# Kernel optimization log

Measured on AMD Instinct MI355X. Metric: run time of the kernel, lower is better.

The kernel has to match this reference:

```python
import jax, jax.numpy as jnp
import numpy as np

B, S, D = 4, 2048, 768
H, E = 12, 64  # num_heads, head_size


def setup_inputs() -> dict:
    key = jax.random.key(0)
    ks = jax.random.split(key, 9)
    sd = 1.0 / np.sqrt(D)
    return {
        "x": jax.random.normal(ks[0], (B, S, D), dtype=jnp.float32),
        "Wq": jax.random.normal(ks[1], (H, D, E), dtype=jnp.float32) * sd,
        "bq": jax.random.normal(ks[2], (H, E), dtype=jnp.float32) * 0.02,
        "Wk": jax.random.normal(ks[3], (H, D, E), dtype=jnp.float32) * sd,
        "bk": jax.random.normal(ks[4], (H, E), dtype=jnp.float32) * 0.02,
        "Wv": jax.random.normal(ks[5], (H, D, E), dtype=jnp.float32) * sd,
        "bv": jax.random.normal(ks[6], (H, E), dtype=jnp.float32) * 0.02,
        "Wp": jax.random.normal(ks[7], (H * E, D), dtype=jnp.float32) * sd,
        "bp": jax.random.normal(ks[8], (D,), dtype=jnp.float32) * 0.02,
    }


def reference(x, Wq, bq, Wk, bk, Wv, bv, Wp, bp):
    # Batched multi-head QKV projections (replaces per-head Python loop)
    q = jnp.einsum("bsd,hde->bhse", x, Wq) + bq[None, :, None, :]
    k = jnp.einsum("bsd,hde->bhse", x, Wk) + bk[None, :, None, :]
    v = jnp.einsum("bsd,hde->bhse", x, Wv) + bv[None, :, None, :]
    scale = 1.0 / jnp.sqrt(jnp.asarray(E, dtype=x.dtype))
    # Full materialized attention matrix [B,H,S,S] as in the original module
    wei = jnp.einsum("bhqe,bhke->bhqk", q, k) * scale
    wei = jax.nn.softmax(wei, axis=-1)  # dropout=0 (eval) => identity
    out = jnp.einsum("bhqk,bhke->bhqe", wei, v)  # [B,H,S,E]
    # concat heads in head order then output projection
    out = out.transpose(0, 2, 1, 3).reshape(B, S, H * E)
    return out @ Wp + bp
```

## Files before the change

kernel.cpp:

```cpp
#include <hip/hip_runtime.h>
#include <cstddef>
#include <cstdint>

#define NB 4
#define NH 12
#define SQ 2048
#define DM 768
#define EH 64
#define MTOT (NB*SQ)
#define NQKV (NH*3*EH)

typedef __attribute__((ext_vector_type(8))) short short8;
typedef __attribute__((ext_vector_type(4))) float floatx4;

#define QSCALE 0.18033688011112042f

__device__ __forceinline__ unsigned short f2bf(float f) {
    unsigned int u = __float_as_uint(f);
    u += 0x7fffu + ((u >> 16) & 1u);
    return (unsigned short)(u >> 16);
}

#if __has_builtin(__builtin_amdgcn_exp2f)
__device__ __forceinline__ float fast_exp2(float x) { return __builtin_amdgcn_exp2f(x); }
#else
__device__ __forceinline__ float fast_exp2(float x) { return exp2f(x); }
#endif

#if __has_builtin(__builtin_amdgcn_cvt_pk_bf16_f32)
typedef __attribute__((ext_vector_type(2))) __bf16 bf16x2_t;
__device__ __forceinline__ unsigned int pack_bf16(float lo, float hi) {
    bf16x2_t v = __builtin_amdgcn_cvt_pk_bf16_f32(lo, hi);
    return __builtin_bit_cast(unsigned int, v);
}
#else
__device__ __forceinline__ unsigned int pack_bf16(float lo, float hi) {
    unsigned int u0 = __float_as_uint(lo) + 0x8000u;
    unsigned int u1 = __float_as_uint(hi) + 0x8000u;
    return __builtin_amdgcn_perm(u1, u0, 0x07060302u);
}
#endif
__device__ __forceinline__ short8 pack8(float a0,float a1,float a2,float a3,
                                        float b0,float b1,float b2,float b3) {
    union { unsigned int u[4]; short8 s; } cv;
    cv.u[0] = pack_bf16(a0, a1);
    cv.u[1] = pack_bf16(a2, a3);
    cv.u[2] = pack_bf16(b0, b1);
    cv.u[3] = pack_bf16(b2, b3);
    return cv.s;
}
__device__ __forceinline__ void gl_lds16(const void* g, void* l) {
    __builtin_amdgcn_global_load_lds(
        (const __attribute__((address_space(1))) unsigned int*)g,
        (__attribute__((address_space(3))) unsigned int*)l, 16, 0, 0);
}

#define CVT_A 1572864
#define CVT_BIAS (CVT_A + 576)
#define NCVT ((CVT_BIAS + 255) / 256)
__global__ __launch_bounds__(256) void convert_all(
    const float* __restrict__ x,
    const float* __restrict__ Wq, const float* __restrict__ bq,
    const float* __restrict__ Wk, const float* __restrict__ bk,
    const float* __restrict__ Wv, const float* __restrict__ bv,
    const float* __restrict__ Wp,
    unsigned short* __restrict__ Xb, unsigned short* __restrict__ Wt,
    unsigned short* __restrict__ Wpt, float* __restrict__ bias_all)
{
    __shared__ unsigned short T[64][66];
    if (blockIdx.x < NCVT) {
        int t = blockIdx.x * 256 + threadIdx.x;
        if (t < CVT_A) {
            float4 v = ((const float4*)x)[t];
            ushort4 r; r.x = f2bf(v.x); r.y = f2bf(v.y); r.z = f2bf(v.z); r.w = f2bf(v.w);
            ((ushort4*)Xb)[t] = r;
        } else if (t < CVT_BIAS) {
            int u = (t - CVT_A) * 4;
            #pragma unroll
            for (int j = 0; j < 4; j++) {
                int n = u + j;
                int h = n / 192, rr = n % 192, wsel = rr >> 6, e = rr & 63;
                const float* bs = (wsel == 0) ? bq : ((wsel == 1) ? bk : bv);
                bias_all[n] = bs[h * EH + e] * ((wsel == 0) ? QSCALE : 1.0f);
            }
        }
        return;
    }
    const int bid = blockIdx.x - NCVT;
    const int t = threadIdx.x;
    const int rr = t >> 2;
    const int c4 = (t & 3) * 16;

    const float* src; int sstride; unsigned short* dst; float sc; int kt;
    if (bid < 432) {
        int j = bid / 12; kt = bid % 12;
        int h = j / 3, wsel = j % 3;
        const float* W = (wsel == 0) ? Wq : ((wsel == 1) ? Wk : Wv);
        src = W + (size_t)h * DM * EH;
        sstride = EH;
        dst = Wt + (size_t)(h * 192 + wsel * 64) * DM;
        sc = (wsel == 0) ? QSCALE : 1.0f;
    } else {
        int u = bid - 432;
        int ni = u / 12; kt = u % 12;
        src = Wp + ni * 64;
        sstride = DM;
        dst = Wpt + (size_t)(ni * 64) * DM;
        sc = 1.0f;
    }

    const float* s = src + (size_t)(kt * 64 + rr) * sstride + c4;
    #pragma unroll
    for (int j = 0; j < 16; j++)
        T[c4 + j][rr] = f2bf(s[j] * sc);
    __syncthreads();
    uint4 d0 = *(uint4*)&T[rr][c4];
    uint4 d1 = *(uint4*)&T[rr][c4 + 8];
    *(uint4*)&dst[(size_t)rr * DM + kt * 64 + c4]     = d0;
    *(uint4*)&dst[(size_t)rr * DM + kt * 64 + c4 + 8] = d1;
}

__global__ __launch_bounds__(256, 4) void qkv_mfma(
    const unsigned short* __restrict__ Xb, const unsigned short* __restrict__ Wt,
    const float* __restrict__ bias_all,
    unsigned short* __restrict__ Qo, unsigned short* __restrict__ Kf,
    unsigned short* __restrict__ Vf)
{
    __shared__ __align__(16) unsigned short SM[16384];
    unsigned short* const As0 = SM;
    unsigned short* const Bs0 = SM + 8192;
    const int tid = threadIdx.x;
    const int w = tid >> 6, lane = tid & 63;
    const int l15 = lane & 15, quad = lane >> 4;
    const int wm = w & 1, wn = w >> 1;
    const int m0 = blockIdx.x * 128, n0 = blockIdx.y * 128;
    const int srow = w * 32 + (lane >> 2);
    const int pchunk = lane & 3;

    floatx4 acc[4][4];
    #pragma unroll
    for (int i = 0; i < 4; i++)
        #pragma unroll
        for (int j = 0; j < 4; j++) acc[i][j] = 0;

    #pragma unroll
    for (int c = 0; c < 2; c++) {
        int mr = srow + c * 16;
        int j = (pchunk - (mr >> 1)) & 3;
        gl_lds16(&Xb[(size_t)(m0 + mr) * DM + j * 8],
                 &As0[w * 1024 + c * 512 + lane * 8]);
        gl_lds16(&Wt[(size_t)(n0 + mr) * DM + j * 8],
                 &Bs0[w * 1024 + c * 512 + lane * 8]);
    }

    for (int kt = 0; kt < DM / 32; kt++) {
        const int cur = kt & 1;
        __syncthreads();
        if (kt + 1 < DM / 32) {
            int k0n = (kt + 1) * 32;
            #pragma unroll
            for (int c = 0; c < 2; c++) {
                int mr = srow + c * 16;
                int j = (pchunk - (mr >> 1)) & 3;
                gl_lds16(&Xb[(size_t)(m0 + mr) * DM + k0n + j * 8],
                         &As0[(cur ^ 1) * 4096 + w * 1024 + c * 512 + lane * 8]);
                gl_lds16(&Wt[(size_t)(n0 + mr) * DM + k0n + j * 8],
                         &Bs0[(cur ^ 1) * 4096 + w * 1024 + c * 512 + lane * 8]);
            }
        }
        short8 af[4], bf[4];
        #pragma unroll
        for (int mi = 0; mi < 4; mi++) {
            int row = wm * 64 + mi * 16 + l15;
            int pp = (quad + (row >> 1)) & 3;
            af[mi] = *(const short8*)&As0[cur * 4096 + row * 32 + pp * 8];
        }
        #pragma unroll
        for (int ni = 0; ni < 4; ni++) {
            int row = wn * 64 + ni * 16 + l15;
            int pp = (quad + (row >> 1)) & 3;
            bf[ni] = *(const short8*)&Bs0[cur * 4096 + row * 32 + pp * 8];
        }
        #pragma unroll
        for (int mi = 0; mi < 4; mi++)
            #pragma unroll
            for (int ni = 0; ni < 4; ni++)
                acc[mi][ni] = __builtin_amdgcn_mfma_f32_16x16x32_bf16(
                    af[mi], bf[ni], acc[mi][ni], 0, 0, 0);
    }
    __syncthreads();

    const int bB = m0 >> 11;
    const int ntb0 = n0 + wn * 64;
    const int h = ntb0 / 192, rr = ntb0 % 192;
    const int wsel = rr >> 6;
    const size_t bhbase = ((size_t)bB * NH + h) * (SQ * EH);
    const int sb_base = (m0 & 2047) + wm * 64;
    unsigned short* Ew = SM + w * 1152;
    float bvv[4];
    #pragma unroll
    for (int ni = 0; ni < 4; ni++) bvv[ni] = bias_all[ntb0 + ni * 16 + l15];

    if (wsel == 0) {
        #pragma unroll
        for (int mi = 0; mi < 4; mi++) {
            #pragma unroll
            for (int ni = 0; ni < 4; ni++)
                #pragma unroll
                for (int r = 0; r < 4; r++)
                    Ew[(quad * 4 + r) * 72 + ni * 16 + l15] =
                        f2bf(acc[mi][ni][r] + bvv[ni]);
            #pragma unroll
            for (int t = 0; t < 2; t++) {
                uint4 d = *(uint4*)&Ew[(t * 8 + (lane >> 3)) * 72 + (lane & 7) * 8];
                *(uint4*)&Qo[bhbase +
                    (size_t)(sb_base + mi * 16 + t * 8 + (lane >> 3)) * EH +
                    (lane & 7) * 8] = d;
            }
        }
    } else if (wsel == 1) {
        size_t tbase = bhbase + (size_t)(sb_base >> 6) * 4096;
        #pragma unroll
        for (int mi = 0; mi < 4; mi++) {
            #pragma unroll
            for (int ni = 0; ni < 4; ni++)
                #pragma unroll
                for (int r = 0; r < 4; r++)
                    Ew[(quad * 4 + r) * 72 + ni * 16 + l15] =
                        f2bf(acc[mi][ni][r] + bvv[ni]);
            #pragma unroll
            for (int t = 0; t < 2; t++) {
                uint4 d = *(uint4*)&Ew[l15 * 72 + t * 32 + quad * 8];
                *(uint4*)&Kf[tbase +
                    (size_t)((mi * 2 + t) * 64 + quad * 16 + l15) * 8] = d;
            }
        }
    } else {
        size_t tbase = bhbase + (size_t)(sb_base >> 6) * 4096;
        #pragma unroll
        for (int ni = 0; ni < 4; ni++) {
            #pragma unroll
            for (int mi = 0; mi < 4; mi++)
                #pragma unroll
                for (int r = 0; r < 4; r += 2) {
                    unsigned int pr = pack_bf16(acc[mi][ni][r]     + bvv[ni],
                                                acc[mi][ni][r + 1] + bvv[ni]);
                    *(unsigned int*)&Ew[l15 * 72 + quad * 16 + mi * 4 + r] = pr;
                }
            #pragma unroll
            for (int t = 0; t < 2; t++) {
                uint4 d = *(uint4*)&Ew[l15 * 72 + t * 32 + quad * 8];
                int unit = (ni * 2 + (quad & 1)) * 64 + ((quad >> 1) + 2 * t) * 16 + l15;
                *(uint4*)&Vf[tbase + (size_t)unit * 8] = d;
            }
        }
    }
}

__global__ __launch_bounds__(256, 3) void attn_mfma(
    const unsigned short* __restrict__ Q, const unsigned short* __restrict__ Kf,
    const unsigned short* __restrict__ Vf, unsigned short* __restrict__ O)
{
    __shared__ unsigned short Ks[3 * 4096];
    __shared__ unsigned short Vs[3 * 4096];
    const int tid = threadIdx.x;
    const int w = tid >> 6, lane = tid & 63;
    const int l15 = lane & 15, quad = lane >> 4;
    const int bh = blockIdx.x;
    const int b = bh / NH, h = bh % NH;
    const int q0 = blockIdx.y * 128;
    const int lin = blockIdx.x + gridDim.x * blockIdx.y;
    const int t0 = (lin >> 8) * 11;

    const unsigned short* Qb = Q + (size_t)bh * SQ * EH;
    const unsigned short* Kb = Kf + (size_t)bh * SQ * EH;
    const unsigned short* Vb = Vf + (size_t)bh * SQ * EH;

    short8 qf[2][2];
    #pragma unroll
    for (int qh = 0; qh < 2; qh++)
        #pragma unroll
        for (int kh = 0; kh < 2; kh++)
            qf[qh][kh] = *(const short8*)
                &Qb[(size_t)(q0 + w * 32 + qh * 16 + l15) * EH + kh * 32 + quad * 8];

    short8 ones;
    #pragma unroll
    for (int j = 0; j < 8; j++) ones[j] = (short)0x3F80;
    const floatx4 fzero = 0;

    floatx4 o[2][4], l_acc[2];
    #pragma unroll
    for (int qh = 0; qh < 2; qh++) {
        l_acc[qh] = 0;
        #pragma unroll
        for (int nb = 0; nb < 4; nb++) o[qh][nb] = 0;
    }

    const int seg = w * 2;
    {
        const unsigned short* K0 = Kb + (size_t)t0 * 4096;
        const unsigned short* V0 = Vb + (size_t)t0 * 4096;
        #pragma unroll
        for (int c = 0; c < 2; c++) {
            gl_lds16(&K0[(seg + c) * 512 + lane * 8], &Ks[(seg + c) * 512 + lane * 8]);
            gl_lds16(&V0[(seg + c) * 512 + lane * 8], &Vs[(seg + c) * 512 + lane * 8]);
        }
    }
    asm volatile("" ::: "memory");
    {
        const int t1 = (t0 + 1) & 31;
        const unsigned short* K1 = Kb + (size_t)t1 * 4096;
        const unsigned short* V1 = Vb + (size_t)t1 * 4096;
        #pragma unroll
        for (int c = 0; c < 2; c++) {
            gl_lds16(&K1[(seg + c) * 512 + lane * 8],
                     &Ks[4096 + (seg + c) * 512 + lane * 8]);
            gl_lds16(&V1[(seg + c) * 512 + lane * 8],
                     &Vs[4096 + (seg + c) * 512 + lane * 8]);
        }
    }
    asm volatile("s_waitcnt vmcnt(4)\n\ts_barrier" ::: "memory");

    int cur_off = 0;
    for (int kb = 0; kb < SQ / 64; kb++) {
        if (kb + 2 < SQ / 64) {
            int nxt_off = cur_off + 8192;
            if (nxt_off >= 12288) nxt_off -= 12288;
            const int tt2 = (t0 + kb + 2) & 31;
            const unsigned short* Kn = Kb + (size_t)tt2 * 4096;
            const unsigned short* Vn = Vb + (size_t)tt2 * 4096;
            #pragma unroll
            for (int c = 0; c < 2; c++) {
                gl_lds16(&Kn[(seg + c) * 512 + lane * 8],
                         &Ks[nxt_off + (seg + c) * 512 + lane * 8]);
                gl_lds16(&Vn[(seg + c) * 512 + lane * 8],
                         &Vs[nxt_off + (seg + c) * 512 + lane * 8]);
            }
        }

        short8 kf[4][2], vf[4][2];
        #pragma unroll
        for (int nb = 0; nb < 4; nb++)
            #pragma unroll
            for (int kh = 0; kh < 2; kh++)
                kf[nb][kh] = *(const short8*)&Ks[cur_off + ((nb * 2 + kh) * 64 + lane) * 8];
        #pragma unroll
        for (int eb = 0; eb < 4; eb++)
            #pragma unroll
            for (int kh = 0; kh < 2; kh++)
                vf[eb][kh] = *(const short8*)&Vs[cur_off + ((eb * 2 + kh) * 64 + lane) * 8];

        floatx4 s[2][4];
        __builtin_amdgcn_s_setprio(1);
        #pragma unroll
        for (int qh = 0; qh < 2; qh++)
            #pragma unroll
            for (int nb = 0; nb < 4; nb++) {
                floatx4 z = __builtin_amdgcn_mfma_f32_16x16x32_bf16(
                    kf[nb][0], qf[qh][0], fzero, 0, 0, 0);
                s[qh][nb] = __builtin_amdgcn_mfma_f32_16x16x32_bf16(
                    kf[nb][1], qf[qh][1], z, 0, 0, 0);
            }
        __builtin_amdgcn_s_setprio(0);

        short8 pa[2][2];
        #pragma unroll
        for (int qh = 0; qh < 2; qh++) {
            float p[4][4];
            #pragma unroll
            for (int nb = 0; nb < 4; nb++)
                #pragma unroll
                for (int r = 0; r < 4; r++)
                    p[nb][r] = fast_exp2(s[qh][nb][r]);
            pa[qh][0] = pack8(p[0][0], p[0][1], p[0][2], p[0][3],
                              p[1][0], p[1][1], p[1][2], p[1][3]);
            pa[qh][1] = pack8(p[2][0], p[2][1], p[2][2], p[2][3],
                              p[3][0], p[3][1], p[3][2], p[3][3]);
        }

        __builtin_amdgcn_s_setprio(1);
        #pragma unroll
        for (int qh = 0; qh < 2; qh++) {
            l_acc[qh] = __builtin_amdgcn_mfma_f32_16x16x32_bf16(pa[qh][0], ones, l_acc[qh], 0, 0, 0);
            l_acc[qh] = __builtin_amdgcn_mfma_f32_16x16x32_bf16(pa[qh][1], ones, l_acc[qh], 0, 0, 0);
        }
        #pragma unroll
        for (int qh = 0; qh < 2; qh++)
            #pragma unroll
            for (int eb = 0; eb < 4; eb++) {
                o[qh][eb] = __builtin_amdgcn_mfma_f32_16x16x32_bf16(pa[qh][0], vf[eb][0], o[qh][eb], 0, 0, 0);
                o[qh][eb] = __builtin_amdgcn_mfma_f32_16x16x32_bf16(pa[qh][1], vf[eb][1], o[qh][eb], 0, 0, 0);
            }
        __builtin_amdgcn_s_setprio(0);

        if (kb + 2 < SQ / 64) {
            asm volatile("s_waitcnt vmcnt(4)\n\ts_barrier" ::: "memory");
        } else if (kb + 1 < SQ / 64) {
            asm volatile("s_waitcnt vmcnt(0)\n\ts_barrier" ::: "memory");
        }
        cur_off += 4096;
        if (cur_off >= 12288) cur_off = 0;
    }

    #pragma unroll
    for (int qh = 0; qh < 2; qh++)
        #pragma unroll
        for (int r = 0; r < 4; r++) {
            float inv = 1.0f / l_acc[qh][r];
            int sidx = q0 + w * 32 + qh * 16 + quad * 4 + r;
            size_t base = (((size_t)b * SQ + sidx) * NH + h) * EH + l15;
            O[base +  0] = f2bf(o[qh][0][r] * inv);
            O[base + 16] = f2bf(o[qh][1][r] * inv);
            O[base + 32] = f2bf(o[qh][2][r] * inv);
            O[base + 48] = f2bf(o[qh][3][r] * inv);
        }
}

__global__ __launch_bounds__(256, 4) void proj_mfma(
    const unsigned short* __restrict__ Ab, const unsigned short* __restrict__ Wpt,
    const float* __restrict__ bp, float* __restrict__ C)
{
    __shared__ __align__(16) unsigned short SM[12288];
    unsigned short* const As0 = SM;
    unsigned short* const Bs0 = SM + 4096;
    const int tid = threadIdx.x;
    const int w = tid >> 6, lane = tid & 63;
    const int l15 = lane & 15, quad = lane >> 4;
    const int wm = w & 1, wn = w >> 1;
    const int m0 = blockIdx.x * 64, n0 = blockIdx.y * 128;
    const int pchunk = lane & 3;

    floatx4 acc[2][4];
    #pragma unroll
    for (int i = 0; i < 2; i++)
        #pragma unroll
        for (int j = 0; j < 4; j++) acc[i][j] = 0;

    {
        int mr = w * 16 + (lane >> 2);
        int j = (pchunk - (mr >> 1)) & 3;
        gl_lds16(&Ab[(size_t)(m0 + mr) * DM + j * 8], &As0[w * 512 + lane * 8]);
    }
    #pragma unroll
    for (int c = 0; c < 2; c++) {
        int nr = w * 32 + c * 16 + (lane >> 2);
        int j = (pchunk - (nr >> 1)) & 3;
        gl_lds16(&Wpt[(size_t)(n0 + nr) * DM + j * 8],
                 &Bs0[w * 1024 + c * 512 + lane * 8]);
    }

    for (int kt = 0; kt < DM / 32; kt++) {
        const int cur = kt & 1;
        __syncthreads();
        if (kt + 1 < DM / 32) {
            int k0n = (kt + 1) * 32;
            {
                int mr = w * 16 + (lane >> 2);
                int j = (pchunk - (mr >> 1)) & 3;
                gl_lds16(&Ab[(size_t)(m0 + mr) * DM + k0n + j * 8],
                         &As0[(cur ^ 1) * 2048 + w * 512 + lane * 8]);
            }
            #pragma unroll
            for (int c = 0; c < 2; c++) {
                int nr = w * 32 + c * 16 + (lane >> 2);
                int j = (pchunk - (nr >> 1)) & 3;
                gl_lds16(&Wpt[(size_t)(n0 + nr) * DM + k0n + j * 8],
                         &Bs0[(cur ^ 1) * 4096 + w * 1024 + c * 512 + lane * 8]);
            }
        }
        short8 af[2], bf[4];
        #pragma unroll
        for (int mi = 0; mi < 2; mi++) {
            int row = wm * 32 + mi * 16 + l15;
            int pp = (quad + (row >> 1)) & 3;
            af[mi] = *(const short8*)&As0[cur * 2048 + row * 32 + pp * 8];
        }
        #pragma unroll
        for (int ni = 0; ni < 4; ni++) {
            int row = wn * 64 + ni * 16 + l15;
            int pp = (quad + (row >> 1)) & 3;
            bf[ni] = *(const short8*)&Bs0[cur * 4096 + row * 32 + pp * 8];
        }
        #pragma unroll
        for (int mi = 0; mi < 2; mi++)
            #pragma unroll
            for (int ni = 0; ni < 4; ni++)
                acc[mi][ni] = __builtin_amdgcn_mfma_f32_16x16x32_bf16(
                    af[mi], bf[ni], acc[mi][ni], 0, 0, 0);
    }
    __syncthreads();

    float* const Ewf = (float*)SM + w * 1088;
    float bvv[4];
    #pragma unroll
    for (int ni = 0; ni < 4; ni++) bvv[ni] = bp[n0 + wn * 64 + ni * 16 + l15];
    #pragma unroll
    for (int mi = 0; mi < 2; mi++) {
        #pragma unroll
        for (int ni = 0; ni < 4; ni++)
            #pragma unroll
            for (int r = 0; r < 4; r++)
                Ewf[(quad * 4 + r) * 68 + ni * 16 + l15] = acc[mi][ni][r] + bvv[ni];
        #pragma unroll
        for (int t = 0; t < 4; t++) {
            float4 d = *(float4*)&Ewf[(t * 4 + quad) * 68 + l15 * 4];
            *(float4*)&C[(size_t)(m0 + wm * 32 + mi * 16 + t * 4 + quad) * DM +
                         n0 + wn * 64 + l15 * 4] = d;
        }
    }
}

extern "C" void kernel_launch(void* const* d_in, const int* in_sizes, int n_in,
                              void* d_out, int out_size, void* d_ws, size_t ws_size,
                              hipStream_t stream) {
    const float* x  = (const float*)d_in[0];
    const float* Wq = (const float*)d_in[1];
    const float* bq = (const float*)d_in[2];
    const float* Wk = (const float*)d_in[3];
    const float* bk = (const float*)d_in[4];
    const float* Wv = (const float*)d_in[5];
    const float* bv = (const float*)d_in[6];
    const float* Wp = (const float*)d_in[7];
    const float* bp = (const float*)d_in[8];
    float* out = (float*)d_out;

    const size_t QKV_ELEMS = (size_t)NB * NH * SQ * EH;
    unsigned short* Qb   = (unsigned short*)d_ws;
    unsigned short* Kfb  = Qb + QKV_ELEMS;
    unsigned short* Vfb  = Kfb + QKV_ELEMS;
    unsigned short* Abuf = Vfb + QKV_ELEMS;
    unsigned short* Xb   = Abuf + QKV_ELEMS;
    unsigned short* Wtb  = Xb + QKV_ELEMS;
    unsigned short* Wptb = Wtb + (size_t)NQKV * DM;
    float* bias_all      = (float*)(Wptb + (size_t)DM * DM);

    convert_all<<<NCVT + 576, 256, 0, stream>>>(
        x, Wq, bq, Wk, bk, Wv, bv, Wp, Xb, Wtb, Wptb, bias_all);
    qkv_mfma<<<dim3(MTOT / 128, NQKV / 128), 256, 0, stream>>>(
        Xb, Wtb, bias_all, Qb, Kfb, Vfb);
    attn_mfma<<<dim3(NB * NH, SQ / 128), 256, 0, stream>>>(Qb, Kfb, Vfb, Abuf);
    proj_mfma<<<dim3(MTOT / 64, DM / 128), 256, 0, stream>>>(Abuf, Wptb, bp, out);
}
```

Baseline: 209.9 us.

## Split attention key range across two wave groups with LDS reduction

Result: slower. 342.2 us (+63.1%).

```diff
diff --git a/kernel.cpp b/kernel.cpp
--- a/kernel.cpp
+++ b/kernel.cpp
@@ -257,20 +257,20 @@
     }
 }
 
-__global__ __launch_bounds__(256, 3) void attn_mfma(
+__global__ __launch_bounds__(512, 4) void attn_mfma(
     const unsigned short* __restrict__ Q, const unsigned short* __restrict__ Kf,
     const unsigned short* __restrict__ Vf, unsigned short* __restrict__ O)
 {
-    __shared__ unsigned short Ks[3 * 4096];
-    __shared__ unsigned short Vs[3 * 4096];
+    __shared__ __align__(16) unsigned short Ks[4 * 4096];
+    __shared__ __align__(16) unsigned short Vs[4 * 4096];
     const int tid = threadIdx.x;
     const int w = tid >> 6, lane = tid & 63;
     const int l15 = lane & 15, quad = lane >> 4;
+    const int wq = w & 3;
+    const int wk = w >> 2;
     const int bh = blockIdx.x;
     const int b = bh / NH, h = bh % NH;
     const int q0 = blockIdx.y * 128;
-    const int lin = blockIdx.x + gridDim.x * blockIdx.y;
-    const int t0 = (lin >> 8) * 11;
 
     const unsigned short* Qb = Q + (size_t)bh * SQ * EH;
     const unsigned short* Kb = Kf + (size_t)bh * SQ * EH;
@@ -282,7 +282,7 @@
         #pragma unroll
         for (int kh = 0; kh < 2; kh++)
             qf[qh][kh] = *(const short8*)
-                &Qb[(size_t)(q0 + w * 32 + qh * 16 + l15) * EH + kh * 32 + quad * 8];
+                &Qb[(size_t)(q0 + wq * 32 + qh * 16 + l15) * EH + kh * 32 + quad * 8];
 
     short8 ones;
     #pragma unroll
@@ -297,59 +297,45 @@
         for (int nb = 0; nb < 4; nb++) o[qh][nb] = 0;
     }
 
-    const int seg = w * 2;
-    {
-        const unsigned short* K0 = Kb + (size_t)t0 * 4096;
-        const unsigned short* V0 = Vb + (size_t)t0 * 4096;
-        #pragma unroll
-        for (int c = 0; c < 2; c++) {
-            gl_lds16(&K0[(seg + c) * 512 + lane * 8], &Ks[(seg + c) * 512 + lane * 8]);
-            gl_lds16(&V0[(seg + c) * 512 + lane * 8], &Vs[(seg + c) * 512 + lane * 8]);
-        }
-    }
-    asm volatile("" ::: "memory");
-    {
-        const int t1 = (t0 + 1) & 31;
-        const unsigned short* K1 = Kb + (size_t)t1 * 4096;
-        const unsigned short* V1 = Vb + (size_t)t1 * 4096;
-        #pragma unroll
-        for (int c = 0; c < 2; c++) {
-            gl_lds16(&K1[(seg + c) * 512 + lane * 8],
-                     &Ks[4096 + (seg + c) * 512 + lane * 8]);
-            gl_lds16(&V1[(seg + c) * 512 + lane * 8],
-                     &Vs[4096 + (seg + c) * 512 + lane * 8]);
-        }
-    }
-    asm volatile("s_waitcnt vmcnt(4)\n\ts_barrier" ::: "memory");
-
-    int cur_off = 0;
-    for (int kb = 0; kb < SQ / 64; kb++) {
-        if (kb + 2 < SQ / 64) {
-            int nxt_off = cur_off + 8192;
-            if (nxt_off >= 12288) nxt_off -= 12288;
-            const int tt2 = (t0 + kb + 2) & 31;
-            const unsigned short* Kn = Kb + (size_t)tt2 * 4096;
-            const unsigned short* Vn = Vb + (size_t)tt2 * 4096;
-            #pragma unroll
-            for (int c = 0; c < 2; c++) {
-                gl_lds16(&Kn[(seg + c) * 512 + lane * 8],
-                         &Ks[nxt_off + (seg + c) * 512 + lane * 8]);
-                gl_lds16(&Vn[(seg + c) * 512 + lane * 8],
-                         &Vs[nxt_off + (seg + c) * 512 + lane * 8]);
-            }
-        }
-
+    auto stage_pair = [&](int tp) {
+        const int tile = tp + wk;
+        const int bn = tile & 3;
+        const int half = wq & 1;
+        if (wq < 2) {
+            const unsigned short* g = Kb + (size_t)tile * 4096;
+            #pragma unroll
+            for (int c = 0; c < 4; c++) {
+                int off = half * 2048 + c * 512 + lane * 8;
+                gl_lds16(&g[off], &Ks[bn * 4096 + off]);
+            }
+        } else {
+            const unsigned short* g = Vb + (size_t)tile * 4096;
+            #pragma unroll
+            for (int c = 0; c < 4; c++) {
+                int off = half * 2048 + c * 512 + lane * 8;
+                gl_lds16(&g[off], &Vs[bn * 4096 + off]);
+            }
+        }
+    };
+
+    stage_pair(0);
+    asm volatile("s_waitcnt vmcnt(0)\n\ts_barrier" ::: "memory");
+
+    for (int j = 0; j < SQ / 128; j++) {
+        if (j + 1 < SQ / 128) stage_pair(2 * j + 2);
+
+        const int co = ((2 * j + wk) & 3) * 4096;
         short8 kf[4][2], vf[4][2];
         #pragma unroll
         for (int nb = 0; nb < 4; nb++)
             #pragma unroll
             for (int kh = 0; kh < 2; kh++)
-                kf[nb][kh] = *(const short8*)&Ks[cur_off + ((nb * 2 + kh) * 64 + lane) * 8];
+                kf[nb][kh] = *(const short8*)&Ks[co + ((nb * 2 + kh) * 64 + lane) * 8];
         #pragma unroll
         for (int eb = 0; eb < 4; eb++)
             #pragma unroll
             for (int kh = 0; kh < 2; kh++)
-                vf[eb][kh] = *(const short8*)&Vs[cur_off + ((eb * 2 + kh) * 64 + lane) * 8];
+                vf[eb][kh] = *(const short8*)&Vs[co + ((eb * 2 + kh) * 64 + lane) * 8];
 
         floatx4 s[2][4];
         __builtin_amdgcn_s_setprio(1);
@@ -394,27 +380,48 @@
             }
         __builtin_amdgcn_s_setprio(0);
 
-        if (kb + 2 < SQ / 64) {
-            asm volatile("s_waitcnt vmcnt(4)\n\ts_barrier" ::: "memory");
-        } else if (kb + 1 < SQ / 64) {
+        if (j + 1 < SQ / 128)
             asm volatile("s_waitcnt vmcnt(0)\n\ts_barrier" ::: "memory");
-        }
-        cur_off += 4096;
-        if (cur_off >= 12288) cur_off = 0;
-    }
-
-    #pragma unroll
-    for (int qh = 0; qh < 2; qh++)
-        #pragma unroll
-        for (int r = 0; r < 4; r++) {
-            float inv = 1.0f / l_acc[qh][r];
-            int sidx = q0 + w * 32 + qh * 16 + quad * 4 + r;
-            size_t base = (((size_t)b * SQ + sidx) * NH + h) * EH + l15;
-            O[base +  0] = f2bf(o[qh][0][r] * inv);
-            O[base + 16] = f2bf(o[qh][1][r] * inv);
-            O[base + 32] = f2bf(o[qh][2][r] * inv);
-            O[base + 48] = f2bf(o[qh][3][r] * inv);
-        }
+    }
+
+    __syncthreads();
+    float* Xo = (float*)Ks;
+    float* Xl = (float*)Vs;
+    if (wk == 1) {
+        float* po = Xo + wq * 2048;
+        float* pl = Xl + wq * 512;
+        #pragma unroll
+        for (int qh = 0; qh < 2; qh++) {
+            #pragma unroll
+            for (int eb = 0; eb < 4; eb++)
+                *(floatx4*)&po[((qh * 4 + eb) * 64 + lane) * 4] = o[qh][eb];
+            *(floatx4*)&pl[(qh * 64 + lane) * 4] = l_acc[qh];
+        }
+    }
+    __syncthreads();
+    if (wk == 0) {
+        float* po = Xo + wq * 2048;
+        float* pl = Xl + wq * 512;
+        #pragma unroll
+        for (int qh = 0; qh < 2; qh++) {
+            #pragma unroll
+            for (int eb = 0; eb < 4; eb++)
+                o[qh][eb] += *(floatx4*)&po[((qh * 4 + eb) * 64 + lane) * 4];
+            l_acc[qh] += *(floatx4*)&pl[(qh * 64 + lane) * 4];
+        }
+        #pragma unroll
+        for (int qh = 0; qh < 2; qh++)
+            #pragma unroll
+            for (int r = 0; r < 4; r++) {
+                float inv = 1.0f / l_acc[qh][r];
+                int sidx = q0 + wq * 32 + qh * 16 + quad * 4 + r;
+                size_t base = (((size_t)b * SQ + sidx) * NH + h) * EH + l15;
+                O[base +  0] = f2bf(o[qh][0][r] * inv);
+                O[base + 16] = f2bf(o[qh][1][r] * inv);
+                O[base + 32] = f2bf(o[qh][2][r] * inv);
+                O[base + 48] = f2bf(o[qh][3][r] * inv);
+            }
+    }
 }
 
 __global__ __launch_bounds__(256, 4) void proj_mfma(
@@ -539,6 +546,6 @@
         x, Wq, bq, Wk, bk, Wv, bv, Wp, Xb, Wtb, Wptb, bias_all);
     qkv_mfma<<<dim3(MTOT / 128, NQKV / 128), 256, 0, stream>>>(
         Xb, Wtb, bias_all, Qb, Kfb, Vfb);
-    attn_mfma<<<dim3(NB * NH, SQ / 128), 256, 0, stream>>>(Qb, Kfb, Vfb, Abuf);
+    attn_mfma<<<dim3(NB * NH, SQ / 128), 512, 0, stream>>>(Qb, Kfb, Vfb, Abuf);
     proj_mfma<<<dim3(MTOT / 64, DM / 128), 256, 0, stream>>>(Abuf, Wptb, bp, out);
 }
```
